# Performance work log

Measured on AMD Instinct MI355X. Metric: run time of the kernel, lower is better.

## Reference

```python
import jax, jax.numpy as jnp
import numpy as np

B, S, J, D = 256, 512, 32, 3
LOG_2PI = float(np.log(2.0 * np.pi))


def setup_inputs() -> dict:
    key = jax.random.key(0)
    k1, k2, k3, k4 = jax.random.split(key, 4)
    y_true = jax.random.normal(k1, (B, S, J, D), dtype=jnp.float32)
    y_pred_mean = jax.random.normal(k2, (B, S, J, D), dtype=jnp.float32)
    # Lower-triangular Cholesky factor with strictly positive diagonal.
    L = jnp.tril(jax.random.uniform(k3, (B, S, J, D, D), dtype=jnp.float32))
    diag = jax.random.uniform(k4, (B, S, J, D), dtype=jnp.float32, minval=0.5, maxval=1.5)
    idx = jnp.arange(D)
    L = L.at[..., idx, idx].set(diag)
    return {"y_true": y_true, "y_pred_mean": y_pred_mean, "pred_cholesky_L": L}


def reference(y_true, y_pred_mean, pred_cholesky_L):
    L = pred_cholesky_L
    # log det Sigma = 2 * sum(log(diag(L)))  -- shape (B,S,J)
    diag = jnp.diagonal(L, axis1=-2, axis2=-1)
    log_det_sigma = 2.0 * jnp.sum(jnp.log(diag), axis=-1)
    # Closed-form forward substitution for the 3x3 lower-triangular solve L x = d
    d = y_true - y_pred_mean
    x0 = d[..., 0] / L[..., 0, 0]
    x1 = (d[..., 1] - L[..., 1, 0] * x0) / L[..., 1, 1]
    x2 = (d[..., 2] - L[..., 2, 0] * x0 - L[..., 2, 1] * x1) / L[..., 2, 2]
    mahalanobis = x0 * x0 + x1 * x1 + x2 * x2  # (B,S,J)
    loss = 0.5 * (mahalanobis + log_det_sigma + D * LOG_2PI)
    return jnp.mean(loss)
```

## Files before the change

### kernel.cpp

```cpp
#include <hip/hip_runtime.h>
#include <math.h>

constexpr int NGROUPS = 256 * 512 * 32;
constexpr int NQUAD   = NGROUPS / 4;
constexpr int BLOCK   = 256;
constexpr int GRID    = 2048;

#define LOG_2PI 1.8378770664093453f

__global__ __launch_bounds__(BLOCK) void nll_main(
    const float* __restrict__ yt,
    const float* __restrict__ yp,
    const float* __restrict__ Lm,
    float* __restrict__ partial)
{
    const float4* yt4 = reinterpret_cast<const float4*>(yt);
    const float4* yp4 = reinterpret_cast<const float4*>(yp);
    const float4* L4  = reinterpret_cast<const float4*>(Lm);

    float acc = 0.0f;
    const int stride = gridDim.x * blockDim.x;
    for (int q = blockIdx.x * blockDim.x + threadIdx.x; q < NQUAD; q += stride) {
        float d[12];
        float l[36];
        #pragma unroll
        for (int i = 0; i < 3; ++i) {
            float4 a = yt4[q * 3 + i];
            float4 b = yp4[q * 3 + i];
            d[i * 4 + 0] = a.x - b.x;
            d[i * 4 + 1] = a.y - b.y;
            d[i * 4 + 2] = a.z - b.z;
            d[i * 4 + 3] = a.w - b.w;
        }
        #pragma unroll
        for (int i = 0; i < 9; ++i) {
            float4 v = L4[q * 9 + i];
            l[i * 4 + 0] = v.x;
            l[i * 4 + 1] = v.y;
            l[i * 4 + 2] = v.z;
            l[i * 4 + 3] = v.w;
        }
        #pragma unroll
        for (int g = 0; g < 4; ++g) {
            float L00 = l[g * 9 + 0];
            float L10 = l[g * 9 + 3];
            float L11 = l[g * 9 + 4];
            float L20 = l[g * 9 + 6];
            float L21 = l[g * 9 + 7];
            float L22 = l[g * 9 + 8];
            float d0 = d[g * 3 + 0];
            float d1 = d[g * 3 + 1];
            float d2 = d[g * 3 + 2];

            float x0 = d0 / L00;
            float x1 = (d1 - L10 * x0) / L11;
            float x2 = (d2 - L20 * x0 - L21 * x1) / L22;
            float maha   = x0 * x0 + x1 * x1 + x2 * x2;
            float logdet = 2.0f * (__logf(L00) + __logf(L11) + __logf(L22));
            acc += 0.5f * (maha + logdet + 3.0f * LOG_2PI);
        }
    }

    #pragma unroll
    for (int off = 32; off > 0; off >>= 1) acc += __shfl_down(acc, off, 64);

    __shared__ float sdata[BLOCK / 64];
    const int lane = threadIdx.x & 63;
    const int wid  = threadIdx.x >> 6;
    if (lane == 0) sdata[wid] = acc;
    __syncthreads();
    if (threadIdx.x == 0) {
        float s = 0.0f;
        #pragma unroll
        for (int w = 0; w < BLOCK / 64; ++w) s += sdata[w];
        partial[blockIdx.x] = s;
    }
}

__global__ __launch_bounds__(256) void nll_reduce(
    const float* __restrict__ partial, float* __restrict__ out)
{
    float acc = 0.0f;
    for (int i = threadIdx.x; i < GRID; i += 256) acc += partial[i];

    #pragma unroll
    for (int off = 32; off > 0; off >>= 1) acc += __shfl_down(acc, off, 64);

    __shared__ float sdata[4];
    const int lane = threadIdx.x & 63;
    const int wid  = threadIdx.x >> 6;
    if (lane == 0) sdata[wid] = acc;
    __syncthreads();
    if (threadIdx.x == 0) {
        out[0] = (sdata[0] + sdata[1] + sdata[2] + sdata[3]) *
                 (1.0f / (float)NGROUPS);
    }
}

extern "C" void kernel_launch(void* const* d_in, const int* in_sizes, int n_in,
                              void* d_out, int out_size, void* d_ws, size_t ws_size,
                              hipStream_t stream)
{
    const float* yt = (const float*)d_in[0];
    const float* yp = (const float*)d_in[1];
    const float* Lm = (const float*)d_in[2];
    float* out      = (float*)d_out;
    float* partial  = (float*)d_ws;

    nll_main<<<GRID, BLOCK, 0, stream>>>(yt, yp, Lm, partial);
    nll_reduce<<<1, 256, 0, stream>>>(partial, out);
}
```

Measured before the change: 43.98 us.

## Use one quad per thread, nontemporal loads, fast reciprocals and hoisted constant

Drops the grid-stride loop so each thread handles exactly one quad, with the grid sized to cover all data (4096 blocks instead of 2048). The y_true and y_pred loads become nontemporal. Divisions are replaced by hardware reciprocal approximations, and the constant log-2π term is folded into the final reduce. The aim is to cut ALU work and improve streaming, at the cost of slightly lower division precision and a larger partial array for the single-block reduce to read.

```diff
diff --git a/kernel.cpp b/kernel.cpp
--- a/kernel.cpp
+++ b/kernel.cpp
@@ -4,9 +4,15 @@
 constexpr int NGROUPS = 256 * 512 * 32;
 constexpr int NQUAD   = NGROUPS / 4;
 constexpr int BLOCK   = 256;
-constexpr int GRID    = 2048;
+constexpr int GRID    = NQUAD / BLOCK;
 
 #define LOG_2PI 1.8378770664093453f
+
+typedef float f32x4 __attribute__((ext_vector_type(4)));
+
+__device__ __forceinline__ float fast_rcp(float x) {
+    return __builtin_amdgcn_rcpf(x);
+}
 
 __global__ __launch_bounds__(BLOCK) void nll_main(
     const float* __restrict__ yt,
@@ -14,51 +20,54 @@
     const float* __restrict__ Lm,
     float* __restrict__ partial)
 {
-    const float4* yt4 = reinterpret_cast<const float4*>(yt);
-    const float4* yp4 = reinterpret_cast<const float4*>(yp);
-    const float4* L4  = reinterpret_cast<const float4*>(Lm);
+    const f32x4* yt4 = reinterpret_cast<const f32x4*>(yt);
+    const f32x4* yp4 = reinterpret_cast<const f32x4*>(yp);
+    const f32x4* L4  = reinterpret_cast<const f32x4*>(Lm);
+
+    const int q = blockIdx.x * BLOCK + threadIdx.x;
+
+    float d[12];
+    #pragma unroll
+    for (int i = 0; i < 3; ++i) {
+        f32x4 a = __builtin_nontemporal_load(&yt4[q * 3 + i]);
+        f32x4 b = __builtin_nontemporal_load(&yp4[q * 3 + i]);
+        d[i * 4 + 0] = a.x - b.x;
+        d[i * 4 + 1] = a.y - b.y;
+        d[i * 4 + 2] = a.z - b.z;
+        d[i * 4 + 3] = a.w - b.w;
+    }
+    float l[36];
+    #pragma unroll
+    for (int i = 0; i < 9; ++i) {
+        f32x4 v = L4[q * 9 + i];
+        l[i * 4 + 0] = v.x;
+        l[i * 4 + 1] = v.y;
+        l[i * 4 + 2] = v.z;
+        l[i * 4 + 3] = v.w;
+    }
 
     float acc = 0.0f;
-    const int stride = gridDim.x * blockDim.x;
-    for (int q = blockIdx.x * blockDim.x + threadIdx.x; q < NQUAD; q += stride) {
-        float d[12];
-        float l[36];
-        #pragma unroll
-        for (int i = 0; i < 3; ++i) {
-            float4 a = yt4[q * 3 + i];
-            float4 b = yp4[q * 3 + i];
-            d[i * 4 + 0] = a.x - b.x;
-            d[i * 4 + 1] = a.y - b.y;
-            d[i * 4 + 2] = a.z - b.z;
-            d[i * 4 + 3] = a.w - b.w;
-        }
-        #pragma unroll
-        for (int i = 0; i < 9; ++i) {
-            float4 v = L4[q * 9 + i];
-            l[i * 4 + 0] = v.x;
-            l[i * 4 + 1] = v.y;
-            l[i * 4 + 2] = v.z;
-            l[i * 4 + 3] = v.w;
-        }
-        #pragma unroll
-        for (int g = 0; g < 4; ++g) {
-            float L00 = l[g * 9 + 0];
-            float L10 = l[g * 9 + 3];
-            float L11 = l[g * 9 + 4];
-            float L20 = l[g * 9 + 6];
-            float L21 = l[g * 9 + 7];
-            float L22 = l[g * 9 + 8];
-            float d0 = d[g * 3 + 0];
-            float d1 = d[g * 3 + 1];
-            float d2 = d[g * 3 + 2];
+    #pragma unroll
+    for (int g = 0; g < 4; ++g) {
+        float L00 = l[g * 9 + 0];
+        float L10 = l[g * 9 + 3];
+        float L11 = l[g * 9 + 4];
+        float L20 = l[g * 9 + 6];
+        float L21 = l[g * 9 + 7];
+        float L22 = l[g * 9 + 8];
+        float d0 = d[g * 3 + 0];
+        float d1 = d[g * 3 + 1];
+        float d2 = d[g * 3 + 2];
 
-            float x0 = d0 / L00;
-            float x1 = (d1 - L10 * x0) / L11;
-            float x2 = (d2 - L20 * x0 - L21 * x1) / L22;
-            float maha   = x0 * x0 + x1 * x1 + x2 * x2;
-            float logdet = 2.0f * (__logf(L00) + __logf(L11) + __logf(L22));
-            acc += 0.5f * (maha + logdet + 3.0f * LOG_2PI);
-        }
+        float r0 = fast_rcp(L00);
+        float r1 = fast_rcp(L11);
+        float r2 = fast_rcp(L22);
+        float x0 = d0 * r0;
+        float x1 = (d1 - L10 * x0) * r1;
+        float x2 = (d2 - L20 * x0 - L21 * x1) * r2;
+        float maha   = x0 * x0 + x1 * x1 + x2 * x2;
+        float logdet = __logf(L00) + __logf(L11) + __logf(L22);
+        acc += 0.5f * maha + logdet;
     }
 
     #pragma unroll
@@ -93,7 +102,8 @@
     __syncthreads();
     if (threadIdx.x == 0) {
         out[0] = (sdata[0] + sdata[1] + sdata[2] + sdata[3]) *
-                 (1.0f / (float)NGROUPS);
+                     (1.0f / (float)NGROUPS) +
+                 0.5f * 3.0f * LOG_2PI;
     }
 }
 
```

Result: slower. 54.67 us (+24.3%).
